# Kernel optimization log

Measured on AMD Instinct MI355X. Metric: run time of the kernel, lower is better.

The kernel has to match this reference:

```python
import jax, jax.numpy as jnp
import numpy as np

N, B, H, L0, L1, C = 196608, 4096, 230, 10, 53, 53


def setup_inputs() -> dict:
    key = jax.random.key(0)
    ks = jax.random.split(key, 12)
    x = jax.random.normal(ks[0], (N, H), jnp.float32)
    label_index = jax.random.randint(ks[1], (N,), 0, C, dtype=jnp.int32)
    rl0 = jax.random.randint(ks[2], (C, 1), 0, L0, dtype=jnp.int32)
    rl1 = jax.random.randint(ks[3], (C, 1), 0, L1, dtype=jnp.int32)
    relation_levels = jnp.concatenate([rl0, rl1], axis=1)  # [C, 2]
    # equal-size bags: 4096 bags of 48 sentences (ragged boundaries)
    scope = (jnp.arange(B + 1, dtype=jnp.int32) * (N // B))
    rel_emb0 = jax.random.normal(ks[4], (L0, H), jnp.float32)
    rel_emb1 = jax.random.normal(ks[5], (L1, H), jnp.float32)
    att_w0 = jax.random.normal(ks[6], (L0,), jnp.float32)
    att_w1 = jax.random.normal(ks[7], (L1,), jnp.float32)
    w_s = jax.random.normal(ks[8], (2, 3 * H), jnp.float32) * 0.05
    b_s = jax.random.normal(ks[9], (2, 1), jnp.float32) * 0.05
    disc_matrix = jax.random.normal(ks[10], (C, 2 * H), jnp.float32) * 0.05
    bias = jnp.zeros((C,), jnp.float32)
    return {"x": x, "rel_emb0": rel_emb0, "rel_emb1": rel_emb1,
            "att_w0": att_w0, "att_w1": att_w1, "w_s": w_s, "b_s": b_s,
            "disc_matrix": disc_matrix, "bias": bias,
            "label_index": label_index, "relation_levels": relation_levels,
            "scope": scope}


def _segment_softmax(logits, seg, num_seg):
    # logits: [N]; stable softmax within each bag (segment)
    m = jax.ops.segment_max(logits, seg, num_segments=num_seg)
    e = jnp.exp(logits - m[seg])
    z = jax.ops.segment_sum(e, seg, num_segments=num_seg)
    return e / z[seg]


def reference(x, rel_emb0, rel_emb1, att_w0, att_w1, w_s, b_s, disc_matrix,
              bias, label_index, relation_levels, scope):
    n, h = x.shape
    num_bags = scope.shape[0] - 1
    # bag id of each sentence from ragged boundaries
    seg = jnp.searchsorted(scope, jnp.arange(n, dtype=scope.dtype), side="right") - 1

    ll = relation_levels[label_index]                 # [N, 2]
    r0 = rel_emb0[ll[:, 0]]                           # [N, H]
    r1 = rel_emb1[ll[:, 1]]                           # [N, H]
    s = jnp.tanh(jnp.concatenate([x, r0, r1], axis=-1))  # [N, 3H]
    logits = w_s @ s.T + b_s                          # [2, N]

    # per-bag ragged softmax over sentences, per hierarchy level
    score = jax.vmap(lambda l: _segment_softmax(l, seg, num_bags))(logits)  # [2, N]

    # vertical (hierarchy) attention: softmax over hier per sentence, mean per bag
    v = jnp.stack([att_w0[ll[:, 0]], att_w1[ll[:, 1]]])  # [2, N]
    vsm = jax.nn.softmax(v, axis=0)                      # [2, N]
    counts = jax.ops.segment_sum(jnp.ones((n,), x.dtype), seg, num_segments=num_bags)
    layer_att = jax.vmap(lambda r: jax.ops.segment_sum(r, seg, num_segments=num_bags))(vsm) / counts  # [2, B]

    # attention-weighted bag representation: per bag, [2, len] @ [len, H]
    rep = jax.vmap(lambda sc: jax.ops.segment_sum(sc[:, None] * x, seg, num_segments=num_bags))(score)  # [2, B, H]
    tower = (layer_att[:, :, None] * rep).transpose(1, 0, 2).reshape(num_bags, 2 * h)  # [B, 2H]

    return tower @ disc_matrix.T + bias  # [B, C]
```

## Files before the change

kernel.cpp:

```cpp
#include <hip/hip_runtime.h>
#include <math.h>

#define NTOT 196608
#define BAGS 4096
#define H 230
#define H3 690
#define NC 53
#define MAXCNT 48

__device__ __forceinline__ float fast_tanh(float x) {
    float e = __expf(2.f * x);
    float r = __builtin_amdgcn_rcpf(e + 1.f);
    return fmaf(-2.f, r, 1.f);
}

__global__ void class_table_kernel(const float* __restrict__ rel_emb0,
                                   const float* __restrict__ rel_emb1,
                                   const float* __restrict__ att_w0,
                                   const float* __restrict__ att_w1,
                                   const float* __restrict__ w_s,
                                   const float* __restrict__ b_s,
                                   const int* __restrict__ relation_levels,
                                   float* __restrict__ cls)
{
    int c = blockIdx.x;
    int lane = threadIdx.x;
    int l0 = relation_levels[c * 2 + 0];
    int l1 = relation_levels[c * 2 + 1];
    float a00 = 0.f, a01 = 0.f, a10 = 0.f, a11 = 0.f;
    for (int j = lane; j < H; j += 64) {
        float t0 = fast_tanh(rel_emb0[l0 * H + j]);
        float t1 = fast_tanh(rel_emb1[l1 * H + j]);
        a00 += w_s[0 * H3 + H + j] * t0;
        a01 += w_s[0 * H3 + 2 * H + j] * t1;
        a10 += w_s[1 * H3 + H + j] * t0;
        a11 += w_s[1 * H3 + 2 * H + j] * t1;
    }
    for (int m = 32; m; m >>= 1) {
        a00 += __shfl_xor(a00, m);
        a01 += __shfl_xor(a01, m);
        a10 += __shfl_xor(a10, m);
        a11 += __shfl_xor(a11, m);
    }
    if (lane == 0) {
        cls[0 * NC + c] = a00 + a01 + b_s[0];
        cls[1 * NC + c] = a10 + a11 + b_s[1];
        float v0 = att_w0[l0], v1 = att_w1[l1];
        float mx = fmaxf(v0, v1);
        float e0 = __expf(v0 - mx), e1 = __expf(v1 - mx);
        float rz = __builtin_amdgcn_rcpf(e0 + e1);
        cls[2 * NC + c] = e0 * rz;
        cls[3 * NC + c] = e1 * rz;
    }
}

__global__ __launch_bounds__(256) void bag_kernel(
    const float* __restrict__ x,
    const float* __restrict__ w_s,
    const float* __restrict__ disc,
    const float* __restrict__ bias,
    const int* __restrict__ label_index,
    const int* __restrict__ scope,
    const float* __restrict__ cls,
    float* __restrict__ out)
{
    __shared__ __align__(16) float xs[MAXCNT * H];
    __shared__ float lg0[MAXCNT], lg1[MAXCNT];
    __shared__ float sc0[MAXCNT], sc1[MAXCNT];
    __shared__ float vs0[MAXCNT], vs1[MAXCNT];
    __shared__ __align__(16) float t01[464];
    __shared__ float laS[2];

    int b = blockIdx.x;
    int start = scope[b];
    int cnt = scope[b + 1] - start;
    int tid = threadIdx.x;

    long long base = (long long)start * H;
    int nelem = cnt * H;
    const float* xbase = x + base;
    if (((base & 3) == 0) && ((nelem & 3) == 0)) {
        const float4* src = (const float4*)xbase;
        float4* dst = (float4*)xs;
        int nv = nelem >> 2;
        for (int v = tid; v < nv; v += 256) dst[v] = src[v];
    } else {
        for (int e = tid; e < nelem; e += 256) xs[e] = xbase[e];
    }

    int wave = tid >> 6;
    int lane = tid & 63;
    float w0r[4], w1r[4];
#pragma unroll
    for (int u = 0; u < 4; ++u) {
        int jj = lane + 64 * u;
        w0r[u] = (jj < H) ? w_s[jj] : 0.f;
        w1r[u] = (jj < H) ? w_s[H3 + jj] : 0.f;
    }
    __syncthreads();

    for (int i = wave; i < cnt; i += 4) {
        float d0 = 0.f, d1 = 0.f;
#pragma unroll
        for (int u = 0; u < 4; ++u) {
            int jj = lane + 64 * u;
            float t = (jj < H) ? fast_tanh(xs[i * H + jj]) : 0.f;
            d0 += w0r[u] * t;
            d1 += w1r[u] * t;
        }
        for (int m = 32; m; m >>= 1) {
            d0 += __shfl_xor(d0, m);
            d1 += __shfl_xor(d1, m);
        }
        if (lane == 0) {
            int c = label_index[start + i];
            lg0[i] = d0 + cls[c];
            lg1[i] = d1 + cls[NC + c];
            vs0[i] = cls[2 * NC + c];
            vs1[i] = cls[3 * NC + c];
        }
    }
    __syncthreads();

    if (wave == 0) {
        bool act = (lane < cnt);
        float l0v = act ? lg0[lane] : -3.0e38f;
        float l1v = act ? lg1[lane] : -3.0e38f;
        float v0 = act ? vs0[lane] : 0.f;
        float v1 = act ? vs1[lane] : 0.f;
        float m0 = l0v, m1 = l1v;
        for (int m = 32; m; m >>= 1) {
            m0 = fmaxf(m0, __shfl_xor(m0, m));
            m1 = fmaxf(m1, __shfl_xor(m1, m));
        }
        float e0 = act ? __expf(l0v - m0) : 0.f;
        float e1 = act ? __expf(l1v - m1) : 0.f;
        float z0 = e0, z1 = e1, sv0 = v0, sv1 = v1;
        for (int m = 32; m; m >>= 1) {
            z0 += __shfl_xor(z0, m);
            z1 += __shfl_xor(z1, m);
            sv0 += __shfl_xor(sv0, m);
            sv1 += __shfl_xor(sv1, m);
        }
        float rz0 = __builtin_amdgcn_rcpf(z0);
        float rz1 = __builtin_amdgcn_rcpf(z1);
        if (act) {
            sc0[lane] = e0 * rz0;
            sc1[lane] = e1 * rz1;
        }
        if (lane == 0) {
            float rc = __builtin_amdgcn_rcpf((float)cnt);
            laS[0] = sv0 * rc;
            laS[1] = sv1 * rc;
        }
    }
    __syncthreads();

    if (tid < H) {
        float a0 = 0.f, a1 = 0.f;
        for (int i = 0; i < cnt; ++i) {
            float v = xs[i * H + tid];
            a0 += sc0[i] * v;
            a1 += sc1[i] * v;
        }
        t01[tid] = laS[0] * a0;
        t01[H + tid] = laS[1] * a1;
    }
    __syncthreads();

    int q = tid & 3;
    int c = tid >> 2;
    if (c < NC) {
        const float4* drow4 = (const float4*)(disc + c * (2 * H));
        const float4* t4 = (const float4*)t01;
        float acc = 0.f;
        for (int k = q; k < 115; k += 4) {
            float4 dv = drow4[k];
            float4 tv = t4[k];
            acc += dv.x * tv.x + dv.y * tv.y + dv.z * tv.z + dv.w * tv.w;
        }
        acc += __shfl_down(acc, 2, 4);
        acc += __shfl_down(acc, 1, 4);
        if (q == 0) out[b * NC + c] = acc + bias[c];
    }
}

extern "C" void kernel_launch(void* const* d_in, const int* in_sizes, int n_in,
                              void* d_out, int out_size, void* d_ws, size_t ws_size,
                              hipStream_t stream) {
    const float* x               = (const float*)d_in[0];
    const float* rel_emb0        = (const float*)d_in[1];
    const float* rel_emb1        = (const float*)d_in[2];
    const float* att_w0          = (const float*)d_in[3];
    const float* att_w1          = (const float*)d_in[4];
    const float* w_s             = (const float*)d_in[5];
    const float* b_s             = (const float*)d_in[6];
    const float* disc            = (const float*)d_in[7];
    const float* bias            = (const float*)d_in[8];
    const int*   label_index     = (const int*)d_in[9];
    const int*   relation_levels = (const int*)d_in[10];
    const int*   scope           = (const int*)d_in[11];
    float* out = (float*)d_out;
    float* cls = (float*)d_ws;

    class_table_kernel<<<NC, 64, 0, stream>>>(rel_emb0, rel_emb1, att_w0, att_w1,
                                              w_s, b_s, relation_levels, cls);
    bag_kernel<<<BAGS, 256, 0, stream>>>(x, w_s, disc, bias, label_index, scope,
                                         cls, out);
}
```

Baseline: 370.8 us.

## Drop shared-memory x staging; stream rows from global with batched wave reductions

Removes the ~44KB shared buffer for the bag's x rows. Both the tanh-logit pass and the weighted-sum pass now read x straight from global memory, relying on L2/cache for the second read. Logits for six rows per wave are batched so their shuffle reductions interleave. The weighted sum is split across all four waves with a shared partial reduction, and label/class lookups move into the softmax wave. The aim is higher occupancy (launch bounds 256,8) and more memory-level parallelism, at the cost of reading x twice from global and hardcoding at most 48 rows per bag.

```diff
diff --git a/kernel.cpp b/kernel.cpp
--- a/kernel.cpp
+++ b/kernel.cpp
@@ -1,12 +1,10 @@
 #include <hip/hip_runtime.h>
-#include <math.h>
 
 #define NTOT 196608
 #define BAGS 4096
 #define H 230
 #define H3 690
 #define NC 53
-#define MAXCNT 48
 
 __device__ __forceinline__ float fast_tanh(float x) {
     float e = __expf(2.f * x);
@@ -54,7 +52,7 @@
     }
 }
 
-__global__ __launch_bounds__(256) void bag_kernel(
+__global__ __launch_bounds__(256, 8) void bag_kernel(
     const float* __restrict__ x,
     const float* __restrict__ w_s,
     const float* __restrict__ disc,
@@ -64,10 +62,9 @@
     const float* __restrict__ cls,
     float* __restrict__ out)
 {
-    __shared__ __align__(16) float xs[MAXCNT * H];
-    __shared__ float lg0[MAXCNT], lg1[MAXCNT];
-    __shared__ float sc0[MAXCNT], sc1[MAXCNT];
-    __shared__ float vs0[MAXCNT], vs1[MAXCNT];
+    __shared__ float lg0[64], lg1[64];
+    __shared__ float sc0[64], sc1[64];
+    __shared__ __align__(16) float part[4][464];
     __shared__ __align__(16) float t01[464];
     __shared__ float laS[2];
 
@@ -75,21 +72,10 @@
     int start = scope[b];
     int cnt = scope[b + 1] - start;
     int tid = threadIdx.x;
-
-    long long base = (long long)start * H;
-    int nelem = cnt * H;
-    const float* xbase = x + base;
-    if (((base & 3) == 0) && ((nelem & 3) == 0)) {
-        const float4* src = (const float4*)xbase;
-        float4* dst = (float4*)xs;
-        int nv = nelem >> 2;
-        for (int v = tid; v < nv; v += 256) dst[v] = src[v];
-    } else {
-        for (int e = tid; e < nelem; e += 256) xs[e] = xbase[e];
-    }
-
     int wave = tid >> 6;
     int lane = tid & 63;
+    const float* xb = x + (long long)start * H;
+
     float w0r[4], w1r[4];
 #pragma unroll
     for (int u = 0; u < 4; ++u) {
@@ -97,37 +83,56 @@
         w0r[u] = (jj < H) ? w_s[jj] : 0.f;
         w1r[u] = (jj < H) ? w_s[H3 + jj] : 0.f;
     }
-    __syncthreads();
-
-    for (int i = wave; i < cnt; i += 4) {
-        float d0 = 0.f, d1 = 0.f;
-#pragma unroll
-        for (int u = 0; u < 4; ++u) {
-            int jj = lane + 64 * u;
-            float t = (jj < H) ? fast_tanh(xs[i * H + jj]) : 0.f;
-            d0 += w0r[u] * t;
-            d1 += w1r[u] * t;
-        }
+
+#pragma unroll
+    for (int b0 = 0; b0 < 12; b0 += 6) {
+        float d0[6], d1[6];
+#pragma unroll
+        for (int k = 0; k < 6; ++k) { d0[k] = 0.f; d1[k] = 0.f; }
+#pragma unroll
+        for (int k = 0; k < 6; ++k) {
+            int i = wave + 4 * (b0 + k);
+            if (i < cnt) {
+                const float* row = xb + i * H;
+#pragma unroll
+                for (int u = 0; u < 4; ++u) {
+                    int jj = lane + 64 * u;
+                    if (jj < H) {
+                        float t = fast_tanh(row[jj]);
+                        d0[k] += w0r[u] * t;
+                        d1[k] += w1r[u] * t;
+                    }
+                }
+            }
+        }
+#pragma unroll
         for (int m = 32; m; m >>= 1) {
-            d0 += __shfl_xor(d0, m);
-            d1 += __shfl_xor(d1, m);
+#pragma unroll
+            for (int k = 0; k < 6; ++k) {
+                d0[k] += __shfl_xor(d0[k], m);
+                d1[k] += __shfl_xor(d1[k], m);
+            }
         }
         if (lane == 0) {
-            int c = label_index[start + i];
-            lg0[i] = d0 + cls[c];
-            lg1[i] = d1 + cls[NC + c];
-            vs0[i] = cls[2 * NC + c];
-            vs1[i] = cls[3 * NC + c];
+#pragma unroll
+            for (int k = 0; k < 6; ++k) {
+                int i = wave + 4 * (b0 + k);
+                if (i < cnt) { lg0[i] = d0[k]; lg1[i] = d1[k]; }
+            }
         }
     }
     __syncthreads();
 
     if (wave == 0) {
         bool act = (lane < cnt);
-        float l0v = act ? lg0[lane] : -3.0e38f;
-        float l1v = act ? lg1[lane] : -3.0e38f;
-        float v0 = act ? vs0[lane] : 0.f;
-        float v1 = act ? vs1[lane] : 0.f;
+        float l0v = -3.0e38f, l1v = -3.0e38f, v0 = 0.f, v1 = 0.f;
+        if (act) {
+            int c = label_index[start + lane];
+            l0v = lg0[lane] + cls[c];
+            l1v = lg1[lane] + cls[NC + c];
+            v0 = cls[2 * NC + c];
+            v1 = cls[3 * NC + c];
+        }
         float m0 = l0v, m1 = l1v;
         for (int m = 32; m; m >>= 1) {
             m0 = fmaxf(m0, __shfl_xor(m0, m));
@@ -156,15 +161,39 @@
     }
     __syncthreads();
 
-    if (tid < H) {
-        float a0 = 0.f, a1 = 0.f;
-        for (int i = 0; i < cnt; ++i) {
-            float v = xs[i * H + tid];
-            a0 += sc0[i] * v;
-            a1 += sc1[i] * v;
-        }
-        t01[tid] = laS[0] * a0;
-        t01[H + tid] = laS[1] * a1;
+    {
+        float a0[4] = {0.f, 0.f, 0.f, 0.f};
+        float a1[4] = {0.f, 0.f, 0.f, 0.f};
+        for (int t2 = 0; t2 < 12; ++t2) {
+            int i = wave + 4 * t2;
+            if (i < cnt) {
+                float s0 = sc0[i], s1 = sc1[i];
+                const float* row = xb + i * H;
+#pragma unroll
+                for (int u = 0; u < 4; ++u) {
+                    int jj = lane + 64 * u;
+                    if (jj < H) {
+                        float v = row[jj];
+                        a0[u] += s0 * v;
+                        a1[u] += s1 * v;
+                    }
+                }
+            }
+        }
+#pragma unroll
+        for (int u = 0; u < 4; ++u) {
+            int jj = lane + 64 * u;
+            if (jj < H) {
+                part[wave][jj] = a0[u];
+                part[wave][H + jj] = a1[u];
+            }
+        }
+    }
+    __syncthreads();
+
+    for (int t = tid; t < 2 * H; t += 256) {
+        float s = part[0][t] + part[1][t] + part[2][t] + part[3][t];
+        t01[t] = s * laS[t < H ? 0 : 1];
     }
     __syncthreads();
 
```

Measured after the change: 325.6 us. 1.14x faster.

## Stream bag rows once with fused online softmax and weighted accumulation

Applied to the files above, without the earlier changes.

Each bag's sentence rows are no longer staged in LDS. Each wave now reads its rows straight from global memory, computes the tanh logits, and immediately adds exp-weighted rows into per-lane registers. The per-wave partial sums and normalizers are combined through a small shared buffer. This drops the max-subtraction pass and the serial per-column reduction. It also cuts LDS use from about 44KB so more blocks fit per CU, with launch bounds asking for 8. In exchange the softmax is no longer max-stabilized, which relies on the logits staying small enough for exp not to overflow, and the loop is hard-capped at 48 sentences per bag.

```diff
diff --git a/kernel.cpp b/kernel.cpp
--- a/kernel.cpp
+++ b/kernel.cpp
@@ -1,12 +1,10 @@
 #include <hip/hip_runtime.h>
-#include <math.h>
 
 #define NTOT 196608
 #define BAGS 4096
 #define H 230
 #define H3 690
 #define NC 53
-#define MAXCNT 48
 
 __device__ __forceinline__ float fast_tanh(float x) {
     float e = __expf(2.f * x);
@@ -54,7 +52,7 @@
     }
 }
 
-__global__ __launch_bounds__(256) void bag_kernel(
+__global__ __launch_bounds__(256, 8) void bag_kernel(
     const float* __restrict__ x,
     const float* __restrict__ w_s,
     const float* __restrict__ disc,
@@ -64,32 +62,18 @@
     const float* __restrict__ cls,
     float* __restrict__ out)
 {
-    __shared__ __align__(16) float xs[MAXCNT * H];
-    __shared__ float lg0[MAXCNT], lg1[MAXCNT];
-    __shared__ float sc0[MAXCNT], sc1[MAXCNT];
-    __shared__ float vs0[MAXCNT], vs1[MAXCNT];
+    __shared__ __align__(16) float part[4][464];
+    __shared__ float zs[4][4];
     __shared__ __align__(16) float t01[464];
-    __shared__ float laS[2];
 
     int b = blockIdx.x;
     int start = scope[b];
     int cnt = scope[b + 1] - start;
     int tid = threadIdx.x;
-
-    long long base = (long long)start * H;
-    int nelem = cnt * H;
-    const float* xbase = x + base;
-    if (((base & 3) == 0) && ((nelem & 3) == 0)) {
-        const float4* src = (const float4*)xbase;
-        float4* dst = (float4*)xs;
-        int nv = nelem >> 2;
-        for (int v = tid; v < nv; v += 256) dst[v] = src[v];
-    } else {
-        for (int e = tid; e < nelem; e += 256) xs[e] = xbase[e];
-    }
-
     int wave = tid >> 6;
     int lane = tid & 63;
+    const float* xb = x + (long long)start * H;
+
     float w0r[4], w1r[4];
 #pragma unroll
     for (int u = 0; u < 4; ++u) {
@@ -97,74 +81,71 @@
         w0r[u] = (jj < H) ? w_s[jj] : 0.f;
         w1r[u] = (jj < H) ? w_s[H3 + jj] : 0.f;
     }
-    __syncthreads();
 
-    for (int i = wave; i < cnt; i += 4) {
+    float acc0[4] = {0.f, 0.f, 0.f, 0.f};
+    float acc1[4] = {0.f, 0.f, 0.f, 0.f};
+    float z0 = 0.f, z1 = 0.f, sv0 = 0.f, sv1 = 0.f;
+
+    for (int t = 0; t < 12; ++t) {
+        int i = wave + 4 * t;
+        if (i >= cnt) break;
+        const float* row = xb + i * H;
+        float r[4];
         float d0 = 0.f, d1 = 0.f;
 #pragma unroll
         for (int u = 0; u < 4; ++u) {
             int jj = lane + 64 * u;
-            float t = (jj < H) ? fast_tanh(xs[i * H + jj]) : 0.f;
-            d0 += w0r[u] * t;
-            d1 += w1r[u] * t;
+            r[u] = (jj < H) ? row[jj] : 0.f;
         }
+#pragma unroll
+        for (int u = 0; u < 4; ++u) {
+            float tnh = fast_tanh(r[u]);
+            d0 += w0r[u] * tnh;
+            d1 += w1r[u] * tnh;
+        }
+#pragma unroll
         for (int m = 32; m; m >>= 1) {
             d0 += __shfl_xor(d0, m);
             d1 += __shfl_xor(d1, m);
         }
-        if (lane == 0) {
-            int c = label_index[start + i];
-            lg0[i] = d0 + cls[c];
-            lg1[i] = d1 + cls[NC + c];
-            vs0[i] = cls[2 * NC + c];
-            vs1[i] = cls[3 * NC + c];
+        int c = label_index[start + i];
+        float e0 = __expf(d0 + cls[c]);
+        float e1 = __expf(d1 + cls[NC + c]);
+        z0 += e0; z1 += e1;
+        sv0 += cls[2 * NC + c];
+        sv1 += cls[3 * NC + c];
+#pragma unroll
+        for (int u = 0; u < 4; ++u) {
+            acc0[u] = fmaf(e0, r[u], acc0[u]);
+            acc1[u] = fmaf(e1, r[u], acc1[u]);
         }
+    }
+
+#pragma unroll
+    for (int u = 0; u < 4; ++u) {
+        int jj = lane + 64 * u;
+        if (jj < H) {
+            part[wave][jj]     = acc0[u];
+            part[wave][H + jj] = acc1[u];
+        }
+    }
+    if (lane == 0) {
+        zs[wave][0] = z0; zs[wave][1] = z1;
+        zs[wave][2] = sv0; zs[wave][3] = sv1;
     }
     __syncthreads();
 
-    if (wave == 0) {
-        bool act = (lane < cnt);
-        float l0v = act ? lg0[lane] : -3.0e38f;
-        float l1v = act ? lg1[lane] : -3.0e38f;
-        float v0 = act ? vs0[lane] : 0.f;
-        float v1 = act ? vs1[lane] : 0.f;
-        float m0 = l0v, m1 = l1v;
-        for (int m = 32; m; m >>= 1) {
-            m0 = fmaxf(m0, __shfl_xor(m0, m));
-            m1 = fmaxf(m1, __shfl_xor(m1, m));
-        }
-        float e0 = act ? __expf(l0v - m0) : 0.f;
-        float e1 = act ? __expf(l1v - m1) : 0.f;
-        float z0 = e0, z1 = e1, sv0 = v0, sv1 = v1;
-        for (int m = 32; m; m >>= 1) {
-            z0 += __shfl_xor(z0, m);
-            z1 += __shfl_xor(z1, m);
-            sv0 += __shfl_xor(sv0, m);
-            sv1 += __shfl_xor(sv1, m);
-        }
-        float rz0 = __builtin_amdgcn_rcpf(z0);
-        float rz1 = __builtin_amdgcn_rcpf(z1);
-        if (act) {
-            sc0[lane] = e0 * rz0;
-            sc1[lane] = e1 * rz1;
-        }
-        if (lane == 0) {
-            float rc = __builtin_amdgcn_rcpf((float)cnt);
-            laS[0] = sv0 * rc;
-            laS[1] = sv1 * rc;
-        }
-    }
-    __syncthreads();
+    float zt0 = zs[0][0] + zs[1][0] + zs[2][0] + zs[3][0];
+    float zt1 = zs[0][1] + zs[1][1] + zs[2][1] + zs[3][1];
+    float st0 = zs[0][2] + zs[1][2] + zs[2][2] + zs[3][2];
+    float st1 = zs[0][3] + zs[1][3] + zs[2][3] + zs[3][3];
+    float rc  = __builtin_amdgcn_rcpf((float)cnt);
+    float s0  = st0 * rc * __builtin_amdgcn_rcpf(zt0);
+    float s1  = st1 * rc * __builtin_amdgcn_rcpf(zt1);
 
-    if (tid < H) {
-        float a0 = 0.f, a1 = 0.f;
-        for (int i = 0; i < cnt; ++i) {
-            float v = xs[i * H + tid];
-            a0 += sc0[i] * v;
-            a1 += sc1[i] * v;
-        }
-        t01[tid] = laS[0] * a0;
-        t01[H + tid] = laS[1] * a1;
+    for (int t = tid; t < 2 * H; t += 256) {
+        float s = part[0][t] + part[1][t] + part[2][t] + part[3][t];
+        t01[t] = s * (t < H ? s0 : s1);
     }
     __syncthreads();
 
```

After: 301.0 us. 1.23x faster.

## Split logit dot products by column chunk per wave, drop softmax max pass

Applied to the files above, without the earlier changes.

Logit computation now gives each lane one sentence row and each wave a 58-column slice, with partial sums combined through shared memory. This removes the per-sentence wave-wide shuffle reductions. The softmax skips max subtraction and folds the normalization into the per-bag layer scale. Dropping the max makes exp overflow possible for large logits, and row-wise LDS access with stride 230 may cause bank conflicts.

```diff
diff --git a/kernel.cpp b/kernel.cpp
--- a/kernel.cpp
+++ b/kernel.cpp
@@ -1,12 +1,12 @@
 #include <hip/hip_runtime.h>
-#include <math.h>
 
 #define NTOT 196608
 #define BAGS 4096
 #define H 230
 #define H3 690
 #define NC 53
-#define MAXCNT 48
+#define MAXC 48
+#define HS 58
 
 __device__ __forceinline__ float fast_tanh(float x) {
     float e = __expf(2.f * x);
@@ -64,10 +64,10 @@
     const float* __restrict__ cls,
     float* __restrict__ out)
 {
-    __shared__ __align__(16) float xs[MAXCNT * H];
-    __shared__ float lg0[MAXCNT], lg1[MAXCNT];
-    __shared__ float sc0[MAXCNT], sc1[MAXCNT];
-    __shared__ float vs0[MAXCNT], vs1[MAXCNT];
+    __shared__ __align__(16) float xs[MAXC * H];
+    __shared__ __align__(16) float2 wsl[232];
+    __shared__ float part_d[4][2][64];
+    __shared__ __align__(8) float2 scp[64];
     __shared__ __align__(16) float t01[464];
     __shared__ float laS[2];
 
@@ -75,96 +75,100 @@
     int start = scope[b];
     int cnt = scope[b + 1] - start;
     int tid = threadIdx.x;
-
-    long long base = (long long)start * H;
+    int wave = tid >> 6;
+    int lane = tid & 63;
+    const float* xb = x + (long long)start * H;
+
+    if (tid < H) wsl[tid] = make_float2(w_s[tid], w_s[H3 + tid]);
+
     int nelem = cnt * H;
-    const float* xbase = x + base;
-    if (((base & 3) == 0) && ((nelem & 3) == 0)) {
-        const float4* src = (const float4*)xbase;
+    if ((((unsigned long long)(uintptr_t)xb & 15ull) == 0) && ((nelem & 3) == 0)) {
+        const float4* src = (const float4*)xb;
         float4* dst = (float4*)xs;
         int nv = nelem >> 2;
         for (int v = tid; v < nv; v += 256) dst[v] = src[v];
     } else {
-        for (int e = tid; e < nelem; e += 256) xs[e] = xbase[e];
-    }
-
-    int wave = tid >> 6;
-    int lane = tid & 63;
-    float w0r[4], w1r[4];
-#pragma unroll
-    for (int u = 0; u < 4; ++u) {
-        int jj = lane + 64 * u;
-        w0r[u] = (jj < H) ? w_s[jj] : 0.f;
-        w1r[u] = (jj < H) ? w_s[H3 + jj] : 0.f;
-    }
-    __syncthreads();
-
-    for (int i = wave; i < cnt; i += 4) {
-        float d0 = 0.f, d1 = 0.f;
-#pragma unroll
-        for (int u = 0; u < 4; ++u) {
-            int jj = lane + 64 * u;
-            float t = (jj < H) ? fast_tanh(xs[i * H + jj]) : 0.f;
-            d0 += w0r[u] * t;
-            d1 += w1r[u] * t;
-        }
-        for (int m = 32; m; m >>= 1) {
-            d0 += __shfl_xor(d0, m);
-            d1 += __shfl_xor(d1, m);
-        }
-        if (lane == 0) {
-            int c = label_index[start + i];
-            lg0[i] = d0 + cls[c];
-            lg1[i] = d1 + cls[NC + c];
-            vs0[i] = cls[2 * NC + c];
-            vs1[i] = cls[3 * NC + c];
-        }
+        for (int e = tid; e < nelem; e += 256) xs[e] = xb[e];
+    }
+    __syncthreads();
+
+    {
+        int j0 = wave * HS;
+        int j1 = j0 + HS; if (j1 > H) j1 = H;
+        float d0a = 0.f, d0b = 0.f, d1a = 0.f, d1b = 0.f;
+        if (lane < cnt) {
+            const float* row = xs + lane * H;
+#pragma unroll 4
+            for (int j = j0; j < j1; j += 2) {
+                float2 wa = wsl[j];
+                float2 wb = wsl[j + 1];
+                float xa = row[j];
+                float xb2 = row[j + 1];
+                float ta = fast_tanh(xa);
+                float tb = fast_tanh(xb2);
+                d0a = fmaf(wa.x, ta, d0a);
+                d1a = fmaf(wa.y, ta, d1a);
+                d0b = fmaf(wb.x, tb, d0b);
+                d1b = fmaf(wb.y, tb, d1b);
+            }
+        }
+        part_d[wave][0][lane] = d0a + d0b;
+        part_d[wave][1][lane] = d1a + d1b;
     }
     __syncthreads();
 
     if (wave == 0) {
         bool act = (lane < cnt);
-        float l0v = act ? lg0[lane] : -3.0e38f;
-        float l1v = act ? lg1[lane] : -3.0e38f;
-        float v0 = act ? vs0[lane] : 0.f;
-        float v1 = act ? vs1[lane] : 0.f;
-        float m0 = l0v, m1 = l1v;
-        for (int m = 32; m; m >>= 1) {
-            m0 = fmaxf(m0, __shfl_xor(m0, m));
-            m1 = fmaxf(m1, __shfl_xor(m1, m));
-        }
-        float e0 = act ? __expf(l0v - m0) : 0.f;
-        float e1 = act ? __expf(l1v - m1) : 0.f;
-        float z0 = e0, z1 = e1, sv0 = v0, sv1 = v1;
+        float e0 = 0.f, e1 = 0.f, v0 = 0.f, v1 = 0.f;
+        if (act) {
+            float d0 = part_d[0][0][lane] + part_d[1][0][lane]
+                     + part_d[2][0][lane] + part_d[3][0][lane];
+            float d1 = part_d[0][1][lane] + part_d[1][1][lane]
+                     + part_d[2][1][lane] + part_d[3][1][lane];
+            int c = label_index[start + lane];
+            e0 = __expf(d0 + cls[c]);
+            e1 = __expf(d1 + cls[NC + c]);
+            v0 = cls[2 * NC + c];
+            v1 = cls[3 * NC + c];
+        }
+        scp[lane] = make_float2(e0, e1);
+        float z0 = e0, z1 = e1;
+#pragma unroll
         for (int m = 32; m; m >>= 1) {
             z0 += __shfl_xor(z0, m);
             z1 += __shfl_xor(z1, m);
-            sv0 += __shfl_xor(sv0, m);
-            sv1 += __shfl_xor(sv1, m);
-        }
-        float rz0 = __builtin_amdgcn_rcpf(z0);
-        float rz1 = __builtin_amdgcn_rcpf(z1);
-        if (act) {
-            sc0[lane] = e0 * rz0;
-            sc1[lane] = e1 * rz1;
+            v0 += __shfl_xor(v0, m);
+            v1 += __shfl_xor(v1, m);
         }
         if (lane == 0) {
             float rc = __builtin_amdgcn_rcpf((float)cnt);
-            laS[0] = sv0 * rc;
-            laS[1] = sv1 * rc;
+            laS[0] = v0 * rc * __builtin_amdgcn_rcpf(z0);
+            laS[1] = v1 * rc * __builtin_amdgcn_rcpf(z1);
         }
     }
     __syncthreads();
 
     if (tid < H) {
-        float a0 = 0.f, a1 = 0.f;
-        for (int i = 0; i < cnt; ++i) {
-            float v = xs[i * H + tid];
-            a0 += sc0[i] * v;
-            a1 += sc1[i] * v;
-        }
-        t01[tid] = laS[0] * a0;
-        t01[H + tid] = laS[1] * a1;
+        float a0 = 0.f, a1 = 0.f, b0 = 0.f, b1 = 0.f;
+        int i = 0;
+        for (; i + 1 < cnt; i += 2) {
+            float2 sa = scp[i];
+            float2 sb = scp[i + 1];
+            float va = xs[i * H + tid];
+            float vb = xs[(i + 1) * H + tid];
+            a0 = fmaf(sa.x, va, a0);
+            a1 = fmaf(sa.y, va, a1);
+            b0 = fmaf(sb.x, vb, b0);
+            b1 = fmaf(sb.y, vb, b1);
+        }
+        if (i < cnt) {
+            float2 sa = scp[i];
+            float va = xs[i * H + tid];
+            a0 = fmaf(sa.x, va, a0);
+            a1 = fmaf(sa.y, va, a1);
+        }
+        t01[tid]     = (a0 + b0) * laS[0];
+        t01[H + tid] = (a1 + b1) * laS[1];
     }
     __syncthreads();
 
```

Result: faster. 340.1 us (-8.3%).
